# Optimization experiments

Measured on AMD Instinct MI355X. Metric: run time of the kernel, lower is better.

## Reference

```python
import jax, jax.numpy as jnp
import numpy as np
from jax import lax

DN = ('NCHW', 'OIHW', 'NCHW')
EPS = 1e-5

def conv2d(x, w):
    return lax.conv_general_dilated(x, w, (1, 1), 'VALID', dimension_numbers=DN)

def bn(x, g, b, m, v):
    # eval-mode BatchNorm2d, params shape [C]
    scale = (g / jnp.sqrt(v + EPS))[None, :, None, None]
    shift = (b - m * g / jnp.sqrt(v + EPS))[None, :, None, None]
    return x * scale + shift

def xcorr_depthwise(search, kernel):
    # search [B,C,Hs,Ws], kernel [B,C,hk,wk] -> [B,C,Hs-hk+1,Ws-wk+1]
    B, C, Hs, Ws = search.shape
    hk, wk = kernel.shape[2], kernel.shape[3]
    s = search.reshape(1, B * C, Hs, Ws)
    k = kernel.reshape(B * C, 1, hk, wk)
    out = lax.conv_general_dilated(s, k, (1, 1), 'VALID',
                                   dimension_numbers=DN,
                                   feature_group_count=B * C)
    return out.reshape(B, C, Hs - hk + 1, Ws - wk + 1)

def _bn_params(key, c):
    k1, k2, k3, k4 = jax.random.split(key, 4)
    g = jax.random.uniform(k1, (c,), jnp.float32, 0.5, 1.5)
    b = jax.random.normal(k2, (c,), jnp.float32) * 0.1
    m = jax.random.normal(k3, (c,), jnp.float32) * 0.1
    v = jax.random.uniform(k4, (c,), jnp.float32, 0.5, 1.5)
    return g, b, m, v

def setup_inputs() -> dict:
    key = jax.random.key(0)
    ks = jax.random.split(key, 10)
    IN, H, OUT = 256, 256, 10
    kernel = jax.random.normal(ks[0], (128, IN, 7, 7), jnp.float32)
    search = jax.random.normal(ks[1], (128, IN, 31, 31), jnp.float32)
    w_ck = jax.random.normal(ks[2], (H, IN, 3, 3), jnp.float32) * 0.05
    g1, b1, m1, v1 = _bn_params(ks[3], H)
    w_cs = jax.random.normal(ks[4], (H, IN, 3, 3), jnp.float32) * 0.05
    g2, b2, m2, v2 = _bn_params(ks[5], H)
    w_h1 = jax.random.normal(ks[6], (H, H, 1, 1), jnp.float32) * 0.05
    g3, b3, m3, v3 = _bn_params(ks[7], H)
    w_h2 = jax.random.normal(ks[8], (OUT, H, 1, 1), jnp.float32) * 0.05
    b_h2 = jax.random.normal(ks[9], (OUT,), jnp.float32) * 0.05
    return dict(kernel=kernel, search=search, w_ck=w_ck, g1=g1, b1=b1, m1=m1, v1=v1,
                w_cs=w_cs, g2=g2, b2=b2, m2=m2, v2=v2,
                w_h1=w_h1, g3=g3, b3=b3, m3=m3, v3=v3, w_h2=w_h2, b_h2=b_h2)

def reference(kernel, search, w_ck, g1, b1, m1, v1, w_cs, g2, b2, m2, v2,
              w_h1, g3, b3, m3, v3, w_h2, b_h2):
    # conv_kernel / conv_search branches: Conv3x3 -> BN -> ReLU
    k = jax.nn.relu(bn(conv2d(kernel, w_ck), g1, b1, m1, v1))   # [B,256,5,5]
    s = jax.nn.relu(bn(conv2d(search, w_cs), g2, b2, m2, v2))   # [B,256,29,29]
    # depthwise cross-correlation (search_crop/search_pos are None -> kernel_t = kernel)
    feat = xcorr_depthwise(s, k)                                 # [B,256,25,25]
    # head: Conv1x1 -> BN -> ReLU -> Conv1x1(+bias)
    h = jax.nn.relu(bn(conv2d(feat, w_h1), g3, b3, m3, v3))
    out = conv2d(h, w_h2) + b_h2[None, :, None, None]            # [B,10,25,25]
    return out
```

## Files before the change

### kernel.cpp

```cpp
#include <hip/hip_runtime.h>
#include <hip/hip_bf16.h>

#define EPS 1e-5f

typedef __attribute__((ext_vector_type(8))) short bf16x8;
typedef __attribute__((ext_vector_type(4))) float f32x4;
typedef __attribute__((ext_vector_type(4))) unsigned short u16x4;
typedef __attribute__((ext_vector_type(8))) unsigned short u16x8;

#define WAITVM8 asm volatile("s_waitcnt vmcnt(8)" ::: "memory")
#define WAITVM4 asm volatile("s_waitcnt vmcnt(4)" ::: "memory")
#define WAITVM0 asm volatile("s_waitcnt vmcnt(0)" ::: "memory")
#define BAR()   __builtin_amdgcn_s_barrier()

__device__ __forceinline__ void gld_lds16(const void* g, void* l) {
    __builtin_amdgcn_global_load_lds(
        (const __attribute__((address_space(1))) unsigned int*)g,
        (__attribute__((address_space(3))) unsigned int*)l, 16, 0, 0);
}

#define RD8(RA, RB, SEL) do {                                                  \
    const int _b = (SEL) * 8192;                                               \
    _Pragma("unroll") for (int _i = 0; _i < 4; ++_i)                           \
        RA[_i] = *reinterpret_cast<const bf16x8*>(&lA[_b + aoff + _i * 512]);  \
    _Pragma("unroll") for (int _j = 0; _j < 4; ++_j)                           \
        RB[_j] = *reinterpret_cast<const bf16x8*>(&lB[_b + boff + _j * 512]);  \
} while (0)

#define RD4(RA4, SEL) do {                                                     \
    const int _b = (SEL) * 8192;                                               \
    _Pragma("unroll") for (int _i = 0; _i < 4; ++_i)                           \
        RA4[_i] = *reinterpret_cast<const bf16x8*>(                            \
            &lA[_b + aoff + (_i + 4) * 512]);                                  \
} while (0)

#define MFQ(RA, RB, I0) do {                                                   \
    _Pragma("unroll") for (int _i = 0; _i < 4; ++_i)                           \
    _Pragma("unroll") for (int _j = 0; _j < 4; ++_j)                           \
        acc[(I0) + _i][_j] = __builtin_amdgcn_mfma_f32_16x16x32_bf16(          \
            RA[_i], RB[_j], acc[(I0) + _i][_j], 0, 0, 0);                      \
} while (0)

#define STEP(CA0, CA4, CB, NA0, NB, SELT, STAGE_STMT, WAIT_STMT, DORD) do {    \
    RD4(CA4, (SELT));                                                          \
    STAGE_STMT;                                                                \
    __builtin_amdgcn_s_setprio(1); MFQ(CA0, CB, 0);                            \
    __builtin_amdgcn_s_setprio(0);                                             \
    WAIT_STMT;                                                                 \
    BAR();                                                                     \
    if (DORD) RD8(NA0, NB, ((SELT) + 1) & 3);                                  \
    __builtin_amdgcn_s_setprio(1); MFQ(CA4, CB, 4);                            \
    __builtin_amdgcn_s_setprio(0);                                             \
} while (0)

template<int HIN, int WIN, int NTOT>
__device__ __forceinline__ void conv_dev(
    int bid, int tid,
    __hip_bfloat16* lA, __hip_bfloat16* lB,
    const __hip_bfloat16* __restrict__ xt,
    const __hip_bfloat16* __restrict__ wt,
    const float* __restrict__ g, const float* __restrict__ bb,
    const float* __restrict__ mm_, const float* __restrict__ vv,
    __hip_bfloat16* __restrict__ y)
{
    constexpr int HOUT = HIN - 2, WOUT = WIN - 2, POUT = HOUT * WOUT;
    const int n0  = bid * 256;
    const int wid = tid >> 6, lane = tid & 63;
    const int wr = wid >> 2, wc = wid & 3;

    const int arow = tid >> 2;
    const int seg  = (tid & 3) ^ ((tid >> 3) & 3);

    const size_t wbase0 = (size_t)arow * 2304 + seg * 8;
    const size_t wbase1 = (size_t)(arow + 128) * 2304 + seg * 8;

    int nr0 = n0 + arow;       if (nr0 > NTOT - 1) nr0 = NTOT - 1;
    int nr1 = n0 + arow + 128; if (nr1 > NTOT - 1) nr1 = NTOT - 1;
    int b0 = nr0 / POUT, p0 = nr0 % POUT, oy0 = p0 / WOUT, ox0 = p0 % WOUT;
    int b1 = nr1 / POUT, p1 = nr1 % POUT, oy1 = p1 / WOUT, ox1 = p1 % WOUT;
    const size_t xbase0 = (((size_t)b0 * HIN + oy0) * WIN + ox0) * 256 + seg * 8;
    const size_t xbase1 = (((size_t)b1 * HIN + oy1) * WIN + ox1) * 256 + seg * 8;

    auto stage = [&](int c0, int j, int sel) {
        char* a0 = (char*)lA + sel * 16384 + wid * 1024;
        char* b0p = (char*)lB + sel * 16384 + wid * 1024;
        const int woff = j * 256 + c0;
        gld_lds16(wt + wbase0 + woff, a0);
        gld_lds16(wt + wbase1 + woff, a0 + 8192);
        const int xoff = ((j / 3) * WIN + (j % 3)) * 256 + c0;
        gld_lds16(xt + xbase0 + xoff, b0p);
        gld_lds16(xt + xbase1 + xoff, b0p + 8192);
    };

    f32x4 acc[8][4];
#pragma unroll
    for (int i = 0; i < 8; ++i)
#pragma unroll
        for (int j = 0; j < 4; ++j)
            acc[i][j] = f32x4{0.f, 0.f, 0.f, 0.f};

    const int l15 = lane & 15, l16 = lane >> 4;
    const int slot = l16 ^ ((l15 >> 1) & 3);
    const int aoff = (wr * 128 + l15) * 32 + slot * 8;
    const int boff = (wc * 64  + l15) * 32 + slot * 8;

    bf16x8 pA0[4], pA4[4], pB[4], qA0[4], qA4[4], qB[4];

    stage(0, 0, 0); stage(0, 1, 1); stage(0, 2, 2);
    int js = 3, c0s = 0;
    WAITVM8; BAR();
    RD8(pA0, pB, 0);

#define ADVC do { ++js; if (js == 9) { js = 0; c0s += 32; } } while (0)
    for (int tt = 0; tt < 17; ++tt) {
        STEP(pA0, pA4, pB, qA0, qB, 0, stage(c0s, js, 3), WAITVM8, true); ADVC;
        STEP(qA0, qA4, qB, pA0, pB, 1, stage(c0s, js, 0), WAITVM8, true); ADVC;
        STEP(pA0, pA4, pB, qA0, qB, 2, stage(c0s, js, 1), WAITVM8, true); ADVC;
        STEP(qA0, qA4, qB, pA0, pB, 3, stage(c0s, js, 2), WAITVM8, true); ADVC;
    }
    STEP(pA0, pA4, pB, qA0, qB, 0, stage(c0s, js, 3), WAITVM8, true);
    STEP(qA0, qA4, qB, pA0, pB, 1, (void)0,           WAITVM4, true);
    STEP(pA0, pA4, pB, qA0, qB, 2, (void)0,           WAITVM0, true);
    STEP(qA0, qA4, qB, pA0, pB, 3, (void)0,           (void)0, false);
#undef ADVC

#pragma unroll
    for (int i = 0; i < 8; ++i) {
        const int co_b = wr * 128 + i * 16 + l16 * 4;
        float sc[4], sh[4];
#pragma unroll
        for (int r = 0; r < 4; ++r) {
            sc[r] = g[co_b + r] * rsqrtf(vv[co_b + r] + EPS);
            sh[r] = bb[co_b + r] - mm_[co_b + r] * sc[r];
        }
#pragma unroll
        for (int jj = 0; jj < 4; ++jj) {
            const int n = n0 + wc * 64 + jj * 16 + l15;
            if (n < NTOT) {
                u16x4 o;
#pragma unroll
                for (int r = 0; r < 4; ++r) {
                    const float v = fmaxf(fmaf(acc[i][jj][r], sc[r], sh[r]), 0.f);
                    __hip_bfloat16 hv = __float2bfloat16(v);
                    o[r] = *reinterpret_cast<unsigned short*>(&hv);
                }
                *reinterpret_cast<u16x4*>(&y[(size_t)n * 256 + co_b]) = o;
            }
        }
    }
}

__global__ __launch_bounds__(512, 2) void conv_both(
    const __hip_bfloat16* __restrict__ xt_s, const __hip_bfloat16* __restrict__ wt_cs,
    const float* __restrict__ g2, const float* __restrict__ b2,
    const float* __restrict__ m2, const float* __restrict__ v2,
    __hip_bfloat16* __restrict__ y2,
    const __hip_bfloat16* __restrict__ xt_k, const __hip_bfloat16* __restrict__ wt_ck,
    const float* __restrict__ g1, const float* __restrict__ b1,
    const float* __restrict__ m1, const float* __restrict__ v1,
    __hip_bfloat16* __restrict__ y1)
{
    __shared__ __align__(16) __hip_bfloat16 lA[4 * 8192];
    __shared__ __align__(16) __hip_bfloat16 lB[4 * 8192];
    if (blockIdx.x < 421)
        conv_dev<31, 31, 107648>(blockIdx.x, threadIdx.x, lA, lB,
                                 xt_s, wt_cs, g2, b2, m2, v2, y2);
    else
        conv_dev<7, 7, 3200>(blockIdx.x - 421, threadIdx.x, lA, lB,
                             xt_k, wt_ck, g1, b1, m1, v1, y1);
}

__device__ __forceinline__ void nhwc_body(
    const float* __restrict__ x, __hip_bfloat16* __restrict__ xt, int P,
    int bx, int b, float* t )
{
    const int p0 = bx * 32;
    const float* xb = x + (size_t)b * 256 * P;
    const int pl = threadIdx.x & 31, cg = threadIdx.x >> 5;
#pragma unroll
    for (int it = 0; it < 32; ++it) {
        int c = cg + it * 8, p = p0 + pl;
        t[c * 33 + pl] = (p < P) ? xb[(size_t)c * P + p] : 0.f;
    }
    __syncthreads();
    const int p = threadIdx.x >> 3, l8 = threadIdx.x & 7;
    if (p0 + p < P) {
        __hip_bfloat16* xo = xt + ((size_t)b * P + p0 + p) * 256;
#pragma unroll
        for (int j = 0; j < 4; ++j) {
            const int c0 = j * 64 + l8 * 8;
            u16x8 o;
#pragma unroll
            for (int r = 0; r < 8; ++r) {
                __hip_bfloat16 hv = __float2bfloat16(t[(c0 + r) * 33 + p]);
                o[r] = *reinterpret_cast<unsigned short*>(&hv);
            }
            *reinterpret_cast<u16x8*>(&xo[c0]) = o;
        }
    }
}

__global__ __launch_bounds__(256) void prepass(
    const float* __restrict__ w_ck, __hip_bfloat16* __restrict__ wt_ck,
    const float* __restrict__ w_cs, __hip_bfloat16* __restrict__ wt_cs,
    const float* __restrict__ w_h1, __hip_bfloat16* __restrict__ wh1,
    const float* __restrict__ kernel, __hip_bfloat16* __restrict__ xt_k,
    const float* __restrict__ search, __hip_bfloat16* __restrict__ xt_s)
{
    __shared__ float t[256 * 33];
    const int bid = blockIdx.x;
    if (bid < 512) {
        const float* w = (bid < 256) ? w_ck : w_cs;
        __hip_bfloat16* wt = (bid < 256) ? wt_ck : wt_cs;
        const int co = bid & 255, ci = threadIdx.x;
        const float* wp = w + (size_t)co * 2304 + (size_t)ci * 9;
        __hip_bfloat16* wo = wt + (size_t)co * 2304 + ci;
#pragma unroll
        for (int j = 0; j < 9; ++j)
            wo[(size_t)j * 256] = __float2bfloat16(wp[j]);
    } else if (bid < 768) {
        const int i = (bid - 512) * 256 + threadIdx.x;
        wh1[i] = __float2bfloat16(w_h1[i]);
    } else if (bid < 1024) {
        const int idx = bid - 768;
        nhwc_body(kernel, xt_k, 49, idx & 1, idx >> 1, t);
    } else {
        const int idx = bid - 1024;
        nhwc_body(search, xt_s, 961, idx % 31, idx / 31, t);
    }
}

__global__ __launch_bounds__(256) void xcorr_strip(
    const __hip_bfloat16* __restrict__ s,
    const __hip_bfloat16* __restrict__ k,
    __hip_bfloat16* __restrict__ f)
{
    const int st = blockIdx.x, b = blockIdx.y, c = threadIdx.x;
    const int py0 = st * 5;
    const __hip_bfloat16* sp = s + (size_t)b * 841 * 256 + c;
    const __hip_bfloat16* kp = k + (size_t)b * 25 * 256 + c;

    float kv[25];
#pragma unroll
    for (int i = 0; i < 25; ++i)
        kv[i] = __bfloat162float(kp[(size_t)i * 256]);

    float acc[5][25];
#pragma unroll
    for (int p = 0; p < 5; ++p)
#pragma unroll
        for (int px = 0; px < 25; ++px) acc[p][px] = 0.f;

#pragma unroll
    for (int r = 0; r < 9; ++r) {
        float srow[29];
        const __hip_bfloat16* srp = sp + (size_t)(py0 + r) * 29 * 256;
#pragma unroll
        for (int rx = 0; rx < 29; ++rx)
            srow[rx] = __bfloat162float(srp[(size_t)rx * 256]);
#pragma unroll
        for (int p = 0; p < 5; ++p) {
            if (r >= p && r - p <= 4) {
                const int ky = r - p;
#pragma unroll
                for (int kx = 0; kx < 5; ++kx) {
                    const float kvv = kv[ky * 5 + kx];
#pragma unroll
                    for (int px = 0; px < 25; ++px)
                        acc[p][px] = fmaf(srow[px + kx], kvv, acc[p][px]);
                }
            }
        }
    }

#pragma unroll
    for (int p = 0; p < 5; ++p) {
        __hip_bfloat16* fp = f + ((size_t)b * 625 + (size_t)(py0 + p) * 25) * 256 + c;
#pragma unroll
        for (int px = 0; px < 25; ++px)
            fp[(size_t)px * 256] = __float2bfloat16(acc[p][px]);
    }
}

__global__ __launch_bounds__(512) void head_fused8(
    const __hip_bfloat16* __restrict__ f,
    const __hip_bfloat16* __restrict__ w1,
    const float* __restrict__ g, const float* __restrict__ bb,
    const float* __restrict__ mm_, const float* __restrict__ vv,
    const float* __restrict__ w2,
    const float* __restrict__ b2v,
    float* __restrict__ out)
{
    constexpr int NTOT = 80000;
    const int n0  = blockIdx.x * 256;
    const int tid = threadIdx.x;
    const int wid = tid >> 6, lane = tid & 63;
    const int wr = wid >> 2, wc = wid & 3;

    __shared__ __align__(16) __hip_bfloat16 lA[4 * 8192];
    __shared__ __align__(16) __hip_bfloat16 lB[4 * 8192];

    const int arow = tid >> 2;
    const int seg  = (tid & 3) ^ ((tid >> 3) & 3);

    const size_t wbase0 = (size_t)arow * 256 + seg * 8;
    const size_t wbase1 = (size_t)(arow + 128) * 256 + seg * 8;
    int nr0 = n0 + arow;       if (nr0 > NTOT - 1) nr0 = NTOT - 1;
    int nr1 = n0 + arow + 128; if (nr1 > NTOT - 1) nr1 = NTOT - 1;
    const size_t xbase0 = (size_t)nr0 * 256 + seg * 8;
    const size_t xbase1 = (size_t)nr1 * 256 + seg * 8;

    auto stage = [&](int c0, int sel) {
        char* a0 = (char*)lA + sel * 16384 + wid * 1024;
        char* b0p = (char*)lB + sel * 16384 + wid * 1024;
        gld_lds16(w1 + wbase0 + c0, a0);
        gld_lds16(w1 + wbase1 + c0, a0 + 8192);
        gld_lds16(f + xbase0 + c0, b0p);
        gld_lds16(f + xbase1 + c0, b0p + 8192);
    };

    f32x4 acc[8][4];
#pragma unroll
    for (int i = 0; i < 8; ++i)
#pragma unroll
        for (int j = 0; j < 4; ++j)
            acc[i][j] = f32x4{0.f, 0.f, 0.f, 0.f};

    const int l15 = lane & 15, l16 = lane >> 4;
    const int slot = l16 ^ ((l15 >> 1) & 3);
    const int aoff = (wr * 128 + l15) * 32 + slot * 8;
    const int boff = (wc * 64  + l15) * 32 + slot * 8;

    bf16x8 pA0[4], pA4[4], pB[4], qA0[4], qA4[4], qB[4];

    stage(0, 0); stage(32, 1); stage(64, 2);
    WAITVM8; BAR();
    RD8(pA0, pB, 0);

    STEP(pA0, pA4, pB, qA0, qB, 0, stage(96, 3),  WAITVM8, true);
    STEP(qA0, qA4, qB, pA0, pB, 1, stage(128, 0), WAITVM8, true);
    STEP(pA0, pA4, pB, qA0, qB, 2, stage(160, 1), WAITVM8, true);
    STEP(qA0, qA4, qB, pA0, pB, 3, stage(192, 2), WAITVM8, true);
    STEP(pA0, pA4, pB, qA0, qB, 0, stage(224, 3), WAITVM8, true);
    STEP(qA0, qA4, qB, pA0, pB, 1, (void)0,       WAITVM4, true);
    STEP(pA0, pA4, pB, qA0, qB, 2, (void)0,       WAITVM0, true);
    STEP(qA0, qA4, qB, pA0, pB, 3, (void)0,       (void)0, false);

    __syncthreads();
    float* lw   = (float*)lA;
    float* lred = (float*)lB;
    for (int t = tid; t < 2560; t += 512) lw[t] = w2[t];
    if (tid < 10) lw[2560 + tid] = b2v[tid];
    __syncthreads();

    float p[4][10];
#pragma unroll
    for (int jj = 0; jj < 4; ++jj)
#pragma unroll
        for (int o = 0; o < 10; ++o) p[jj][o] = 0.f;

#pragma unroll
    for (int i = 0; i < 8; ++i) {
        const int co_b = wr * 128 + i * 16 + l16 * 4;
        float sc[4], sh[4];
#pragma unroll
        for (int r = 0; r < 4; ++r) {
            sc[r] = g[co_b + r] * rsqrtf(vv[co_b + r] + EPS);
            sh[r] = bb[co_b + r] - mm_[co_b + r] * sc[r];
        }
        float w4[10][4];
#pragma unroll
        for (int o = 0; o < 10; ++o) {
            f32x4 wv = *reinterpret_cast<const f32x4*>(&lw[o * 256 + co_b]);
#pragma unroll
            for (int r = 0; r < 4; ++r) w4[o][r] = wv[r];
        }
#pragma unroll
        for (int jj = 0; jj < 4; ++jj) {
            float hv[4];
#pragma unroll
            for (int r = 0; r < 4; ++r)
                hv[r] = fmaxf(fmaf(acc[i][jj][r], sc[r], sh[r]), 0.f);
#pragma unroll
            for (int o = 0; o < 10; ++o)
#pragma unroll
                for (int r = 0; r < 4; ++r)
                    p[jj][o] = fmaf(hv[r], w4[o][r], p[jj][o]);
        }
    }

#pragma unroll
    for (int jj = 0; jj < 4; ++jj)
#pragma unroll
        for (int o = 0; o < 10; ++o) {
            float v = p[jj][o];
            v += __shfl_xor(v, 16, 64);
            v += __shfl_xor(v, 32, 64);
            p[jj][o] = v;
        }

    if (wr == 0 && l16 == 0) {
#pragma unroll
        for (int jj = 0; jj < 4; ++jj)
#pragma unroll
            for (int o = 0; o < 10; ++o)
                lred[((wc * 4 + jj) * 16 + l15) * 10 + o] = p[jj][o];
    }
    __syncthreads();
    if (wr == 1) {
#pragma unroll
        for (int jj = 0; jj < 4; ++jj) {
            const int n = n0 + wc * 64 + jj * 16 + l15;
            if (n < NTOT) {
                const int bi = n / 625, pp = n % 625;
#pragma unroll
                for (int t = 0; t < 3; ++t) {
                    const int o = l16 + 4 * t;
                    if (o < 10) {
                        float v = p[jj][o]
                                + lred[((wc * 4 + jj) * 16 + l15) * 10 + o]
                                + lw[2560 + o];
                        out[((size_t)bi * 10 + o) * 625 + pp] = v;
                    }
                }
            }
        }
    }
}

extern "C" void kernel_launch(void* const* d_in, const int* in_sizes, int n_in,
                              void* d_out, int out_size, void* d_ws, size_t ws_size,
                              hipStream_t stream) {
    const float* kernel = (const float*)d_in[0];
    const float* search = (const float*)d_in[1];
    const float* w_ck   = (const float*)d_in[2];
    const float* g1 = (const float*)d_in[3];
    const float* b1 = (const float*)d_in[4];
    const float* m1 = (const float*)d_in[5];
    const float* v1 = (const float*)d_in[6];
    const float* w_cs   = (const float*)d_in[7];
    const float* g2 = (const float*)d_in[8];
    const float* b2 = (const float*)d_in[9];
    const float* m2 = (const float*)d_in[10];
    const float* v2 = (const float*)d_in[11];
    const float* w_h1   = (const float*)d_in[12];
    const float* g3 = (const float*)d_in[13];
    const float* b3 = (const float*)d_in[14];
    const float* m3 = (const float*)d_in[15];
    const float* v3 = (const float*)d_in[16];
    const float* w_h2   = (const float*)d_in[17];
    const float* b_h2   = (const float*)d_in[18];

    float* out = (float*)d_out;

    __hip_bfloat16* ws = (__hip_bfloat16*)d_ws;
    __hip_bfloat16* y1    = ws;
    __hip_bfloat16* y2    = ws + (size_t)819200;
    __hip_bfloat16* wt_ck = ws + (size_t)28377088;
    __hip_bfloat16* wt_cs = ws + (size_t)28966912;
    __hip_bfloat16* wh1   = ws + (size_t)29556736;
    __hip_bfloat16* xt_k  = ws + (size_t)29622272;
    __hip_bfloat16* xt_s  = ws + (size_t)31227904;
    __hip_bfloat16* feat  = ws + (size_t)29622272;

    (void)in_sizes; (void)n_in; (void)out_size; (void)ws_size;

    prepass<<<4992, 256, 0, stream>>>(w_ck, wt_ck, w_cs, wt_cs, w_h1, wh1,
                                      kernel, xt_k, search, xt_s);

    conv_both<<<434, 512, 0, stream>>>(xt_s, wt_cs, g2, b2, m2, v2, y2,
                                       xt_k, wt_ck, g1, b1, m1, v1, y1);

    xcorr_strip<<<dim3(5, 128), 256, 0, stream>>>(y2, y1, feat);

    head_fused8<<<313, 512, 0, stream>>>(feat, wh1, g3, b3, m3, v3, w_h2, b_h2, out);
}
```

Baseline: 302.1 us.

## Fuse depthwise xcorr into head GEMM via shared-memory feature tile

Merges the xcorr strip kernel and the 1x1 head GEMM into one kernel. Each block computes a 5-row strip of the correlation for one batch, split across two thread halves (3 rows and 2 rows), writes it to LDS, then runs the MFMA head on that 125-position tile. The only operand streamed from global memory is the weight. This removes the global feature write/read round trip and one launch. In exchange, each block computes a 128-column N tile with 3 padding columns, the xcorr work is split unevenly between the halves, and the large LDS footprint may limit occupancy.

Result: faster. 266.6 us, median of 3 (-11.7%).

```diff
diff --git a/kernel.cpp b/kernel.cpp
--- a/kernel.cpp
+++ b/kernel.cpp
@@ -10,6 +10,7 @@
 
 #define WAITVM8 asm volatile("s_waitcnt vmcnt(8)" ::: "memory")
 #define WAITVM4 asm volatile("s_waitcnt vmcnt(4)" ::: "memory")
+#define WAITVM2 asm volatile("s_waitcnt vmcnt(2)" ::: "memory")
 #define WAITVM0 asm volatile("s_waitcnt vmcnt(0)" ::: "memory")
 #define BAR()   __builtin_amdgcn_s_barrier()
 
@@ -230,60 +231,9 @@
     }
 }
 
-__global__ __launch_bounds__(256) void xcorr_strip(
+__global__ __launch_bounds__(512) void xcorr_head(
     const __hip_bfloat16* __restrict__ s,
     const __hip_bfloat16* __restrict__ k,
-    __hip_bfloat16* __restrict__ f)
-{
-    const int st = blockIdx.x, b = blockIdx.y, c = threadIdx.x;
-    const int py0 = st * 5;
-    const __hip_bfloat16* sp = s + (size_t)b * 841 * 256 + c;
-    const __hip_bfloat16* kp = k + (size_t)b * 25 * 256 + c;
-
-    float kv[25];
-#pragma unroll
-    for (int i = 0; i < 25; ++i)
-        kv[i] = __bfloat162float(kp[(size_t)i * 256]);
-
-    float acc[5][25];
-#pragma unroll
-    for (int p = 0; p < 5; ++p)
-#pragma unroll
-        for (int px = 0; px < 25; ++px) acc[p][px] = 0.f;
-
-#pragma unroll
-    for (int r = 0; r < 9; ++r) {
-        float srow[29];
-        const __hip_bfloat16* srp = sp + (size_t)(py0 + r) * 29 * 256;
-#pragma unroll
-        for (int rx = 0; rx < 29; ++rx)
-            srow[rx] = __bfloat162float(srp[(size_t)rx * 256]);
-#pragma unroll
-        for (int p = 0; p < 5; ++p) {
-            if (r >= p && r - p <= 4) {
-                const int ky = r - p;
-#pragma unroll
-                for (int kx = 0; kx < 5; ++kx) {
-                    const float kvv = kv[ky * 5 + kx];
-#pragma unroll
-                    for (int px = 0; px < 25; ++px)
-                        acc[p][px] = fmaf(srow[px + kx], kvv, acc[p][px]);
-                }
-            }
-        }
-    }
-
-#pragma unroll
-    for (int p = 0; p < 5; ++p) {
-        __hip_bfloat16* fp = f + ((size_t)b * 625 + (size_t)(py0 + p) * 25) * 256 + c;
-#pragma unroll
-        for (int px = 0; px < 25; ++px)
-            fp[(size_t)px * 256] = __float2bfloat16(acc[p][px]);
-    }
-}
-
-__global__ __launch_bounds__(512) void head_fused8(
-    const __hip_bfloat16* __restrict__ f,
     const __hip_bfloat16* __restrict__ w1,
     const float* __restrict__ g, const float* __restrict__ bb,
     const float* __restrict__ mm_, const float* __restrict__ vv,
@@ -291,71 +241,162 @@
     const float* __restrict__ b2v,
     float* __restrict__ out)
 {
-    constexpr int NTOT = 80000;
-    const int n0  = blockIdx.x * 256;
+    const int st = blockIdx.x, b = blockIdx.y;
+    const int py0 = st * 5;
     const int tid = threadIdx.x;
+
+    __shared__ __align__(16) __hip_bfloat16 featL[128 * 264];
+    __shared__ __align__(16) __hip_bfloat16 lA[3 * 8192];
+
+    {
+        const int c = tid & 255, h = tid >> 8;
+        const __hip_bfloat16* sp = s + (size_t)b * 841 * 256 + c;
+        const __hip_bfloat16* kp = k + (size_t)b * 25 * 256 + c;
+        float kv[25];
+#pragma unroll
+        for (int i = 0; i < 25; ++i)
+            kv[i] = __bfloat162float(kp[(size_t)i * 256]);
+
+        if (h == 0) {
+            float acc3[3][25];
+#pragma unroll
+            for (int p = 0; p < 3; ++p)
+#pragma unroll
+                for (int px = 0; px < 25; ++px) acc3[p][px] = 0.f;
+#pragma unroll
+            for (int r = 0; r < 7; ++r) {
+                float srow[29];
+                const __hip_bfloat16* srp = sp + (size_t)(py0 + r) * 29 * 256;
+#pragma unroll
+                for (int rx = 0; rx < 29; ++rx)
+                    srow[rx] = __bfloat162float(srp[(size_t)rx * 256]);
+#pragma unroll
+                for (int p = 0; p < 3; ++p) {
+                    if (r >= p && r - p <= 4) {
+                        const int ky = r - p;
+#pragma unroll
+                        for (int kx = 0; kx < 5; ++kx) {
+                            const float kvv = kv[ky * 5 + kx];
+#pragma unroll
+                            for (int px = 0; px < 25; ++px)
+                                acc3[p][px] = fmaf(srow[px + kx], kvv, acc3[p][px]);
+                        }
+                    }
+                }
+            }
+#pragma unroll
+            for (int p = 0; p < 3; ++p)
+#pragma unroll
+                for (int px = 0; px < 25; ++px)
+                    featL[(p * 25 + px) * 264 + c] = __float2bfloat16(acc3[p][px]);
+        } else {
+            float acc2[2][25];
+#pragma unroll
+            for (int p = 0; p < 2; ++p)
+#pragma unroll
+                for (int px = 0; px < 25; ++px) acc2[p][px] = 0.f;
+#pragma unroll
+            for (int r = 3; r < 9; ++r) {
+                float srow[29];
+                const __hip_bfloat16* srp = sp + (size_t)(py0 + r) * 29 * 256;
+#pragma unroll
+                for (int rx = 0; rx < 29; ++rx)
+                    srow[rx] = __bfloat162float(srp[(size_t)rx * 256]);
+#pragma unroll
+                for (int p = 3; p < 5; ++p) {
+                    if (r >= p && r - p <= 4) {
+                        const int ky = r - p;
+#pragma unroll
+                        for (int kx = 0; kx < 5; ++kx) {
+                            const float kvv = kv[ky * 5 + kx];
+#pragma unroll
+                            for (int px = 0; px < 25; ++px)
+                                acc2[p - 3][px] = fmaf(srow[px + kx], kvv, acc2[p - 3][px]);
+                        }
+                    }
+                }
+            }
+#pragma unroll
+            for (int p = 0; p < 2; ++p)
+#pragma unroll
+                for (int px = 0; px < 25; ++px)
+                    featL[((p + 3) * 25 + px) * 264 + c] = __float2bfloat16(acc2[p][px]);
+        }
+    }
+    __syncthreads();
+
     const int wid = tid >> 6, lane = tid & 63;
     const int wr = wid >> 2, wc = wid & 3;
-
-    __shared__ __align__(16) __hip_bfloat16 lA[4 * 8192];
-    __shared__ __align__(16) __hip_bfloat16 lB[4 * 8192];
-
-    const int arow = tid >> 2;
-    const int seg  = (tid & 3) ^ ((tid >> 3) & 3);
-
-    const size_t wbase0 = (size_t)arow * 256 + seg * 8;
-    const size_t wbase1 = (size_t)(arow + 128) * 256 + seg * 8;
-    int nr0 = n0 + arow;       if (nr0 > NTOT - 1) nr0 = NTOT - 1;
-    int nr1 = n0 + arow + 128; if (nr1 > NTOT - 1) nr1 = NTOT - 1;
-    const size_t xbase0 = (size_t)nr0 * 256 + seg * 8;
-    const size_t xbase1 = (size_t)nr1 * 256 + seg * 8;
-
-    auto stage = [&](int c0, int sel) {
-        char* a0 = (char*)lA + sel * 16384 + wid * 1024;
-        char* b0p = (char*)lB + sel * 16384 + wid * 1024;
-        gld_lds16(w1 + wbase0 + c0, a0);
-        gld_lds16(w1 + wbase1 + c0, a0 + 8192);
-        gld_lds16(f + xbase0 + c0, b0p);
-        gld_lds16(f + xbase1 + c0, b0p + 8192);
-    };
-
-    f32x4 acc[8][4];
-#pragma unroll
-    for (int i = 0; i < 8; ++i)
-#pragma unroll
-        for (int j = 0; j < 4; ++j)
-            acc[i][j] = f32x4{0.f, 0.f, 0.f, 0.f};
-
     const int l15 = lane & 15, l16 = lane >> 4;
+    const int seg  = (lane & 3) ^ ((lane >> 3) & 3);
     const int slot = l16 ^ ((l15 >> 1) & 3);
     const int aoff = (wr * 128 + l15) * 32 + slot * 8;
-    const int boff = (wc * 64  + l15) * 32 + slot * 8;
-
-    bf16x8 pA0[4], pA4[4], pB[4], qA0[4], qA4[4], qB[4];
-
-    stage(0, 0); stage(32, 1); stage(64, 2);
-    WAITVM8; BAR();
-    RD8(pA0, pB, 0);
-
-    STEP(pA0, pA4, pB, qA0, qB, 0, stage(96, 3),  WAITVM8, true);
-    STEP(qA0, qA4, qB, pA0, pB, 1, stage(128, 0), WAITVM8, true);
-    STEP(pA0, pA4, pB, qA0, qB, 2, stage(160, 1), WAITVM8, true);
-    STEP(qA0, qA4, qB, pA0, pB, 3, stage(192, 2), WAITVM8, true);
-    STEP(pA0, pA4, pB, qA0, qB, 0, stage(224, 3), WAITVM8, true);
-    STEP(qA0, qA4, qB, pA0, pB, 1, (void)0,       WAITVM4, true);
-    STEP(pA0, pA4, pB, qA0, qB, 2, (void)0,       WAITVM0, true);
-    STEP(qA0, qA4, qB, pA0, pB, 3, (void)0,       (void)0, false);
+
+    auto stageA = [&](int c0, int sel) {
+        char* dst = (char*)lA + sel * 16384 + wid * 2048;
+        const size_t r0 = (size_t)(wid * 32 + (lane >> 2)) * 256;
+        gld_lds16(w1 + r0 + c0 + seg * 8, dst);
+        gld_lds16(w1 + r0 + 16 * 256 + c0 + seg * 8, dst + 1024);
+    };
+
+    f32x4 acc[8][2];
+#pragma unroll
+    for (int i = 0; i < 8; ++i) {
+        acc[i][0] = f32x4{0.f, 0.f, 0.f, 0.f};
+        acc[i][1] = f32x4{0.f, 0.f, 0.f, 0.f};
+    }
+
+#define RDH(AF, BF, SEL, C0) do {                                              \
+    const int _b = (SEL) * 8192;                                               \
+    _Pragma("unroll") for (int _i = 0; _i < 8; ++_i)                           \
+        AF[_i] = *reinterpret_cast<const bf16x8*>(&lA[_b + aoff + _i * 512]);  \
+    _Pragma("unroll") for (int _j = 0; _j < 2; ++_j)                           \
+        BF[_j] = *reinterpret_cast<const bf16x8*>(                             \
+            &featL[(wc * 32 + _j * 16 + l15) * 264 + (C0) + l16 * 8]);         \
+} while (0)
+
+#define MFH(AF, BF) do {                                                       \
+    __builtin_amdgcn_s_setprio(1);                                             \
+    _Pragma("unroll") for (int _i = 0; _i < 8; ++_i)                           \
+    _Pragma("unroll") for (int _j = 0; _j < 2; ++_j)                           \
+        acc[_i][_j] = __builtin_amdgcn_mfma_f32_16x16x32_bf16(                 \
+            AF[_i], BF[_j], acc[_i][_j], 0, 0, 0);                             \
+    __builtin_amdgcn_s_setprio(0);                                             \
+} while (0)
+
+    {
+        bf16x8 af[8], bf[2];
+        stageA(0, 0); stageA(32, 1);
+        WAITVM2; BAR();
+        RDH(af, bf, 0, 0);   stageA(64, 2);  MFH(af, bf);
+        WAITVM2; BAR();
+        RDH(af, bf, 1, 32);  stageA(96, 0);  MFH(af, bf);
+        WAITVM2; BAR();
+        RDH(af, bf, 2, 64);  stageA(128, 1); MFH(af, bf);
+        WAITVM2; BAR();
+        RDH(af, bf, 0, 96);  stageA(160, 2); MFH(af, bf);
+        WAITVM2; BAR();
+        RDH(af, bf, 1, 128); stageA(192, 0); MFH(af, bf);
+        WAITVM2; BAR();
+        RDH(af, bf, 2, 160); stageA(224, 1); MFH(af, bf);
+        WAITVM2; BAR();
+        RDH(af, bf, 0, 192);                 MFH(af, bf);
+        WAITVM0; BAR();
+        RDH(af, bf, 1, 224);                 MFH(af, bf);
+    }
+#undef RDH
+#undef MFH
 
     __syncthreads();
     float* lw   = (float*)lA;
-    float* lred = (float*)lB;
+    float* lred = lw + 2816;
     for (int t = tid; t < 2560; t += 512) lw[t] = w2[t];
     if (tid < 10) lw[2560 + tid] = b2v[tid];
     __syncthreads();
 
-    float p[4][10];
-#pragma unroll
-    for (int jj = 0; jj < 4; ++jj)
+    float p[2][10];
+#pragma unroll
+    for (int jj = 0; jj < 2; ++jj)
 #pragma unroll
         for (int o = 0; o < 10; ++o) p[jj][o] = 0.f;
 
@@ -376,7 +417,7 @@
             for (int r = 0; r < 4; ++r) w4[o][r] = wv[r];
         }
 #pragma unroll
-        for (int jj = 0; jj < 4; ++jj) {
+        for (int jj = 0; jj < 2; ++jj) {
             float hv[4];
 #pragma unroll
             for (int r = 0; r < 4; ++r)
@@ -390,7 +431,7 @@
     }
 
 #pragma unroll
-    for (int jj = 0; jj < 4; ++jj)
+    for (int jj = 0; jj < 2; ++jj)
 #pragma unroll
         for (int o = 0; o < 10; ++o) {
             float v = p[jj][o];
@@ -401,26 +442,26 @@
 
     if (wr == 0 && l16 == 0) {
 #pragma unroll
-        for (int jj = 0; jj < 4; ++jj)
+        for (int jj = 0; jj < 2; ++jj)
 #pragma unroll
             for (int o = 0; o < 10; ++o)
-                lred[((wc * 4 + jj) * 16 + l15) * 10 + o] = p[jj][o];
+                lred[((wc * 2 + jj) * 16 + l15) * 10 + o] = p[jj][o];
     }
     __syncthreads();
     if (wr == 1) {
 #pragma unroll
-        for (int jj = 0; jj < 4; ++jj) {
-            const int n = n0 + wc * 64 + jj * 16 + l15;
-            if (n < NTOT) {
-                const int bi = n / 625, pp = n % 625;
+        for (int jj = 0; jj < 2; ++jj) {
+            const int n = wc * 32 + jj * 16 + l15;
+            if (n < 125) {
+                const int py = py0 + n / 25, pxc = n % 25;
 #pragma unroll
                 for (int t = 0; t < 3; ++t) {
                     const int o = l16 + 4 * t;
                     if (o < 10) {
                         float v = p[jj][o]
-                                + lred[((wc * 4 + jj) * 16 + l15) * 10 + o]
+                                + lred[((wc * 2 + jj) * 16 + l15) * 10 + o]
                                 + lw[2560 + o];
-                        out[((size_t)bi * 10 + o) * 625 + pp] = v;
+                        out[(((size_t)b * 10 + o) * 25 + py) * 25 + pxc] = v;
                     }
                 }
             }
@@ -461,7 +502,6 @@
     __hip_bfloat16* wh1   = ws + (size_t)29556736;
     __hip_bfloat16* xt_k  = ws + (size_t)29622272;
     __hip_bfloat16* xt_s  = ws + (size_t)31227904;
-    __hip_bfloat16* feat  = ws + (size_t)29622272;
 
     (void)in_sizes; (void)n_in; (void)out_size; (void)ws_size;
 
@@ -471,7 +511,6 @@
     conv_both<<<434, 512, 0, stream>>>(xt_s, wt_cs, g2, b2, m2, v2, y2,
                                        xt_k, wt_ck, g1, b1, m1, v1, y1);
 
-    xcorr_strip<<<dim3(5, 128), 256, 0, stream>>>(y2, y1, feat);
-
-    head_fused8<<<313, 512, 0, stream>>>(feat, wh1, g3, b3, m3, v3, w_h2, b_h2, out);
-}
+    xcorr_head<<<dim3(5, 128), 512, 0, stream>>>(
+        y2, y1, wh1, g3, b3, m3, v3, w_h2, b_h2, out);
+}
```
